# Performance work log

Measured on AMD Instinct MI355X. Metric: run time of the kernel, lower is better.

Reference implementation:

```python
import jax, jax.numpy as jnp
import numpy as np

INTERVAL = 0.5  # voxel_size_ratio
N_RAYS = 131072
M_SAMPLES = 8388608  # ~64 samples per ray on average
ALPHA_INIT = 0.01


def setup_inputs() -> dict:
    key = jax.random.key(0)
    k1, k2, k3 = jax.random.split(key, 3)
    density = jax.random.normal(k1, (M_SAMPLES,), jnp.float32)
    rgb_feat = jax.random.normal(k2, (M_SAMPLES, 3), jnp.float32)  # raw k0 colors
    # act_shift buffer: log(1/(1-alpha_init) - 1)
    shift = jnp.array([np.log(1.0 / (1.0 - ALPHA_INIT) - 1.0)], jnp.float32)
    # sorted ray ids (samples along each ray are contiguous, near->far)
    ray_id = jnp.sort(jax.random.randint(k3, (M_SAMPLES,), 0, N_RAYS)).astype(jnp.int32)
    return {"density": density, "rgb_feat": rgb_feat, "shift": shift,
            "ray_id": ray_id, "N": N_RAYS}


def reference(density, rgb_feat, shift, ray_id, N):
    # Raw2Alpha: alpha = 1 - (1 + exp(density + shift))^(-interval)
    #          = 1 - exp(-softplus(density + shift) * interval)
    sp = jax.nn.softplus(density + shift[0])
    log1ma = -sp * INTERVAL            # log(1 - alpha), exact
    alpha = 1.0 - jnp.exp(log1ma)

    # Alphas2Weights: per-ray exclusive cumulative product of (1 - alpha)
    # done in log space with a segmented exclusive cumsum.
    seg_tot = jax.ops.segment_sum(log1ma, ray_id, num_segments=N)   # [N] log prod per ray
    seg_excl = jnp.cumsum(seg_tot) - seg_tot                        # log prod of previous rays
    within_excl = jnp.cumsum(log1ma) - log1ma - seg_excl[ray_id]    # exclusive within segment
    T = jnp.exp(within_excl)          # transmittance before each sample
    weights = alpha * T               # [M]
    alphainv_last = jnp.exp(seg_tot)  # [N] leftover transmittance per ray

    # composite colors per ray + white-ish background via alphainv_last
    rgb = jax.nn.sigmoid(rgb_feat)
    rgb_marched = jax.ops.segment_sum(weights[:, None] * rgb, ray_id, num_segments=N)
    out = rgb_marched + alphainv_last[:, None]   # [N, 3]
    return weights, alphainv_last, out
```

## Files before the change

kernel.cpp:

```cpp
#include <hip/hip_runtime.h>


__device__ __forceinline__ float fast_sigmoid(float x) {
    return __builtin_amdgcn_rcpf(1.0f + __expf(-x));
}

#define DPP_ADD(x, ctrl, rmask)                                               \
    do {                                                                      \
        int _s = __builtin_amdgcn_update_dpp(0, __float_as_int(x), (ctrl),    \
                                             (rmask), 0xf, true);             \
        (x) += __int_as_float(_s);                                            \
    } while (0)

#define DPP_MUL(x, ctrl, rmask)                                               \
    do {                                                                      \
        int _s = __builtin_amdgcn_update_dpp(0x3f800000, __float_as_int(x),   \
                                             (ctrl), (rmask), 0xf, false);    \
        (x) *= __int_as_float(_s);                                            \
    } while (0)

__device__ __forceinline__ float wave_scan_add(float x) {
    DPP_ADD(x, 0x111, 0xf);
    DPP_ADD(x, 0x112, 0xf);
    DPP_ADD(x, 0x114, 0xf);
    DPP_ADD(x, 0x118, 0xf);
    DPP_ADD(x, 0x142, 0xa);
    DPP_ADD(x, 0x143, 0xc);
    return x;
}

__device__ __forceinline__ float wave_scan_mul(float x) {
    DPP_MUL(x, 0x111, 0xf);
    DPP_MUL(x, 0x112, 0xf);
    DPP_MUL(x, 0x114, 0xf);
    DPP_MUL(x, 0x118, 0xf);
    DPP_MUL(x, 0x142, 0xa);
    DPP_MUL(x, 0x143, 0xc);
    return x;
}

__device__ __forceinline__ float bcast_lane63(float x) {
    return __int_as_float(__builtin_amdgcn_readlane(__float_as_int(x), 63));
}

__global__ __launch_bounds__(256) void seg_starts4_kernel(
    const int4* __restrict__ ray4, int M4, int M, int N,
    const int* __restrict__ ray_id, int* __restrict__ starts)
{
    const int i = blockIdx.x * blockDim.x + threadIdx.x;
    if (i >= M4) return;
    const int4 v = ray4[i];
    const int prev = (i == 0) ? -1 : ray_id[4 * i - 1];
    const int base = 4 * i;
    for (int r = prev + 1; r <= v.x; ++r) starts[r] = base;
    for (int r = v.x + 1;  r <= v.y; ++r) starts[r] = base + 1;
    for (int r = v.y + 1;  r <= v.z; ++r) starts[r] = base + 2;
    for (int r = v.z + 1;  r <= v.w; ++r) starts[r] = base + 3;
    if (i == M4 - 1) {
        int last = v.w;
        for (int j = 4 * M4; j < M; ++j) {
            const int cur = ray_id[j];
            for (int r = last + 1; r <= cur; ++r) starts[r] = j;
            last = cur;
        }
        for (int r = last + 1; r <= N; ++r) starts[r] = M;
    }
}

#define RPW 4

__global__ __launch_bounds__(256, 4) void favor_render_kernel(
    const float* __restrict__ density,
    const float* __restrict__ rgb_feat,
    const float* __restrict__ shift,
    const int*   __restrict__ starts,
    int M, int N,
    float* __restrict__ weights,
    float* __restrict__ alphainv_last,
    float* __restrict__ out3)
{
    const int wave = (blockIdx.x * blockDim.x + threadIdx.x) >> 6;
    const int t    = threadIdx.x & 63;
    const int r0   = wave * RPW;
    if (r0 >= N) return;

    const int bv = starts[min(r0 + t, N)];
    int s[RPW + 1];
    #pragma unroll
    for (int k = 0; k <= RPW; ++k)
        s[k] = __builtin_amdgcn_readlane(bv, k);

    const float sh = shift[0];

    float d0[RPW], r0v[RPW], g0v[RPW], b0v[RPW];
    float d1[RPW], r1v[RPW], g1v[RPW], b1v[RPW];
    #pragma unroll
    for (int j = 0; j < RPW; ++j) {
        const int st = s[j], en = s[j + 1];
        const int c0 = max(min(st + t, en - 1), 0);
        d0[j]  = density[c0];
        r0v[j] = rgb_feat[3 * c0 + 0];
        g0v[j] = rgb_feat[3 * c0 + 1];
        b0v[j] = rgb_feat[3 * c0 + 2];
    }
    #pragma unroll
    for (int j = 0; j < RPW; ++j) {
        const int st = s[j], en = s[j + 1];
        const int c1 = max(min(st + 64 + t, en - 1), 0);
        d1[j]  = density[c1];
        r1v[j] = rgb_feat[3 * c1 + 0];
        g1v[j] = rgb_feat[3 * c1 + 1];
        b1v[j] = rgb_feat[3 * c1 + 2];
    }
    __builtin_amdgcn_sched_barrier(0);

    float carryT[RPW], accR[RPW], accG[RPW], accB[RPW];

    #pragma unroll
    for (int j = 0; j < RPW; ++j) {
        const int st = s[j], en = s[j + 1];
        const bool valid = (st + t) < en;
        const float u = 1.0f + __expf(d0[j] + sh);
        const float a = __builtin_amdgcn_rsqf(u);
        const float m = valid ? a : 1.0f;
        const float S = wave_scan_mul(m);
        carryT[j] = bcast_lane63(S);
        const float w = S * (u * a - 1.0f);
        accR[j] = valid ? w * fast_sigmoid(r0v[j]) : 0.0f;
        accG[j] = valid ? w * fast_sigmoid(g0v[j]) : 0.0f;
        accB[j] = valid ? w * fast_sigmoid(b0v[j]) : 0.0f;
        if (valid) weights[st + t] = w;
    }

    #pragma unroll
    for (int j = 0; j < RPW; ++j) {
        const int st = s[j], en = s[j + 1];
        if (en - st > 64) {
            const int i = st + 64 + t;
            const bool valid = i < en;
            const float u = 1.0f + __expf(d1[j] + sh);
            const float a = __builtin_amdgcn_rsqf(u);
            const float m = valid ? a : 1.0f;
            const float S = wave_scan_mul(m);
            const float tot = bcast_lane63(S);
            const float w = carryT[j] * S * (u * a - 1.0f);
            accR[j] += valid ? w * fast_sigmoid(r1v[j]) : 0.0f;
            accG[j] += valid ? w * fast_sigmoid(g1v[j]) : 0.0f;
            accB[j] += valid ? w * fast_sigmoid(b1v[j]) : 0.0f;
            if (valid) weights[i] = w;
            carryT[j] *= tot;

            for (int base = st + 128; base < en; base += 64) {
                const int ii = base + t;
                const bool v2 = ii < en;
                const int c = min(ii, en - 1);
                const float dd = density[c];
                const float rr = rgb_feat[3 * c + 0];
                const float gg = rgb_feat[3 * c + 1];
                const float bb = rgb_feat[3 * c + 2];
                const float u2 = 1.0f + __expf(dd + sh);
                const float a2 = __builtin_amdgcn_rsqf(u2);
                const float m2 = v2 ? a2 : 1.0f;
                const float S2 = wave_scan_mul(m2);
                const float tot2 = bcast_lane63(S2);
                const float w2 = carryT[j] * S2 * (u2 * a2 - 1.0f);
                if (v2) {
                    weights[ii] = w2;
                    accR[j] += w2 * fast_sigmoid(rr);
                    accG[j] += w2 * fast_sigmoid(gg);
                    accB[j] += w2 * fast_sigmoid(bb);
                }
                carryT[j] *= tot2;
            }
        }
    }

    float tR[RPW], tG[RPW], tB[RPW];
    #pragma unroll
    for (int j = 0; j < RPW; ++j) {
        tR[j] = wave_scan_add(accR[j]);
        tG[j] = wave_scan_add(accG[j]);
        tB[j] = wave_scan_add(accB[j]);
    }
    #pragma unroll
    for (int j = 0; j < RPW; ++j) {
        const float sR = bcast_lane63(tR[j]);
        const float sG = bcast_lane63(tG[j]);
        const float sB = bcast_lane63(tB[j]);
        const int ray = r0 + j;
        if (t == 0 && ray < N) {
            alphainv_last[ray] = carryT[j];
            out3[3 * ray + 0] = sR + carryT[j];
            out3[3 * ray + 1] = sG + carryT[j];
            out3[3 * ray + 2] = sB + carryT[j];
        }
    }
}

extern "C" void kernel_launch(void* const* d_in, const int* in_sizes, int n_in,
                              void* d_out, int out_size, void* d_ws, size_t ws_size,
                              hipStream_t stream) {
    const float* density  = (const float*)d_in[0];
    const float* rgb_feat = (const float*)d_in[1];
    const float* shift    = (const float*)d_in[2];
    const int*   ray_id   = (const int*)d_in[3];

    const int M = in_sizes[0];
    const int N = (out_size - M) / 4;

    float* weights       = (float*)d_out;
    float* alphainv_last = weights + M;
    float* out3          = alphainv_last + N;

    const int block = 256;
    int* starts = (int*)d_ws;

    const int M4 = M >> 2;
    const int grid_starts = (M4 + block - 1) / block;
    seg_starts4_kernel<<<grid_starts, block, 0, stream>>>(
        (const int4*)ray_id, M4, M, N, ray_id, starts);

    const int n_waves = (N + RPW - 1) / RPW;
    const int grid_render = (n_waves * 64 + block - 1) / block;
    favor_render_kernel<<<grid_render, block, 0, stream>>>(
        density, rgb_feat, shift, starts, M, N,
        weights, alphainv_last, out3);
}
```

Measured before the change: 208.5 us.

## Pack second-chunk samples of two rays into one wave using half-wave scans

New measurement: 213.5 us. +2.4%, slower.

```diff
diff --git a/kernel.cpp b/kernel.cpp
--- a/kernel.cpp
+++ b/kernel.cpp
@@ -39,8 +39,20 @@
     return x;
 }
 
+__device__ __forceinline__ float wave_scan_mul_half(float x) {
+    DPP_MUL(x, 0x111, 0xf);
+    DPP_MUL(x, 0x112, 0xf);
+    DPP_MUL(x, 0x114, 0xf);
+    DPP_MUL(x, 0x118, 0xf);
+    DPP_MUL(x, 0x142, 0xa);
+    return x;
+}
+
 __device__ __forceinline__ float bcast_lane63(float x) {
     return __int_as_float(__builtin_amdgcn_readlane(__float_as_int(x), 63));
+}
+__device__ __forceinline__ float bcast_lane31(float x) {
+    return __int_as_float(__builtin_amdgcn_readlane(__float_as_int(x), 31));
 }
 
 __global__ __launch_bounds__(256) void seg_starts4_kernel(
@@ -68,6 +80,7 @@
 }
 
 #define RPW 4
+#define NPAIR (RPW / 2)
 
 __global__ __launch_bounds__(256, 4) void favor_render_kernel(
     const float* __restrict__ density,
@@ -91,9 +104,9 @@
         s[k] = __builtin_amdgcn_readlane(bv, k);
 
     const float sh = shift[0];
+    const bool lowHalf = t < 32;
 
     float d0[RPW], r0v[RPW], g0v[RPW], b0v[RPW];
-    float d1[RPW], r1v[RPW], g1v[RPW], b1v[RPW];
     #pragma unroll
     for (int j = 0; j < RPW; ++j) {
         const int st = s[j], en = s[j + 1];
@@ -103,16 +116,19 @@
         g0v[j] = rgb_feat[3 * c0 + 1];
         b0v[j] = rgb_feat[3 * c0 + 2];
     }
-    #pragma unroll
-    for (int j = 0; j < RPW; ++j) {
-        const int st = s[j], en = s[j + 1];
-        const int c1 = max(min(st + 64 + t, en - 1), 0);
-        d1[j]  = density[c1];
-        r1v[j] = rgb_feat[3 * c1 + 0];
-        g1v[j] = rgb_feat[3 * c1 + 1];
-        b1v[j] = rgb_feat[3 * c1 + 2];
-    }
-    __builtin_amdgcn_sched_barrier(0);
+    float dP[NPAIR], rP[NPAIR], gP[NPAIR], bP[NPAIR];
+    int   iP[NPAIR];
+    #pragma unroll
+    for (int p = 0; p < NPAIR; ++p) {
+        const int idx = lowHalf ? (s[2 * p] + 64 + t) : (s[2 * p + 1] + 32 + t);
+        const int en  = lowHalf ? s[2 * p + 1] : s[2 * p + 2];
+        iP[p] = idx;
+        const int c = max(min(idx, en - 1), 0);
+        dP[p] = density[c];
+        rP[p] = rgb_feat[3 * c + 0];
+        gP[p] = rgb_feat[3 * c + 1];
+        bP[p] = rgb_feat[3 * c + 2];
+    }
 
     float carryT[RPW], accR[RPW], accG[RPW], accB[RPW];
 
@@ -133,27 +149,41 @@
     }
 
     #pragma unroll
+    for (int p = 0; p < NPAIR; ++p) {
+        const int jA = 2 * p, jB = 2 * p + 1;
+        const int en  = lowHalf ? s[jA + 1] : s[jB + 1];
+        const int idx = iP[p];
+        const bool valid = idx < en;
+        const float u = 1.0f + __expf(dP[p] + sh);
+        const float a = __builtin_amdgcn_rsqf(u);
+        const float m = valid ? a : 1.0f;
+        const float S = wave_scan_mul_half(m);
+        const float totA = bcast_lane31(S);
+        const float totB = bcast_lane63(S);
+        const float carrySel = lowHalf ? carryT[jA] : carryT[jB];
+        const float w = carrySel * S * (u * a - 1.0f);
+        const float cR = valid ? w * fast_sigmoid(rP[p]) : 0.0f;
+        const float cG = valid ? w * fast_sigmoid(gP[p]) : 0.0f;
+        const float cB = valid ? w * fast_sigmoid(bP[p]) : 0.0f;
+        accR[jA] += lowHalf ? cR : 0.0f;
+        accG[jA] += lowHalf ? cG : 0.0f;
+        accB[jA] += lowHalf ? cB : 0.0f;
+        accR[jB] += lowHalf ? 0.0f : cR;
+        accG[jB] += lowHalf ? 0.0f : cG;
+        accB[jB] += lowHalf ? 0.0f : cB;
+        if (valid) weights[idx] = w;
+        carryT[jA] *= totA;
+        carryT[jB] *= totB;
+    }
+
+    #pragma unroll
     for (int j = 0; j < RPW; ++j) {
         const int st = s[j], en = s[j + 1];
-        if (en - st > 64) {
-            const int i = st + 64 + t;
-            const bool valid = i < en;
-            const float u = 1.0f + __expf(d1[j] + sh);
-            const float a = __builtin_amdgcn_rsqf(u);
-            const float m = valid ? a : 1.0f;
-            const float S = wave_scan_mul(m);
-            const float tot = bcast_lane63(S);
-            const float w = carryT[j] * S * (u * a - 1.0f);
-            accR[j] += valid ? w * fast_sigmoid(r1v[j]) : 0.0f;
-            accG[j] += valid ? w * fast_sigmoid(g1v[j]) : 0.0f;
-            accB[j] += valid ? w * fast_sigmoid(b1v[j]) : 0.0f;
-            if (valid) weights[i] = w;
-            carryT[j] *= tot;
-
-            for (int base = st + 128; base < en; base += 64) {
-                const int ii = base + t;
-                const bool v2 = ii < en;
-                const int c = min(ii, en - 1);
+        if (en - st > 96) {
+            for (int base = st + 96; base < en; base += 64) {
+                const int i = base + t;
+                const bool v2 = i < en;
+                const int c = min(i, en - 1);
                 const float dd = density[c];
                 const float rr = rgb_feat[3 * c + 0];
                 const float gg = rgb_feat[3 * c + 1];
@@ -165,7 +195,7 @@
                 const float tot2 = bcast_lane63(S2);
                 const float w2 = carryT[j] * S2 * (u2 * a2 - 1.0f);
                 if (v2) {
-                    weights[ii] = w2;
+                    weights[i] = w2;
                     accR[j] += w2 * fast_sigmoid(rr);
                     accG[j] += w2 * fast_sigmoid(gg);
                     accB[j] += w2 * fast_sigmoid(bb);
```

## Process two samples per lane in first 128-sample chunk with single scan

Applied to the files above, without the earlier changes.

Result: no change. 210.8 us (+1.1%).

```diff
diff --git a/kernel.cpp b/kernel.cpp
--- a/kernel.cpp
+++ b/kernel.cpp
@@ -4,6 +4,9 @@
 __device__ __forceinline__ float fast_sigmoid(float x) {
     return __builtin_amdgcn_rcpf(1.0f + __expf(-x));
 }
+
+struct __align__(4) f3 { float x, y, z; };
+struct __align__(4) f2 { float x, y; };
 
 #define DPP_ADD(x, ctrl, rmask)                                               \
     do {                                                                      \
@@ -37,6 +40,12 @@
     DPP_MUL(x, 0x142, 0xa);
     DPP_MUL(x, 0x143, 0xc);
     return x;
+}
+
+__device__ __forceinline__ float dpp_excl_from_incl(float x) {
+    int r = __builtin_amdgcn_update_dpp(0x3f800000, __float_as_int(x),
+                                        0x138, 0xf, 0xf, false);
+    return __int_as_float(r);
 }
 
 __device__ __forceinline__ float bcast_lane63(float x) {
@@ -92,72 +101,66 @@
 
     const float sh = shift[0];
 
-    float d0[RPW], r0v[RPW], g0v[RPW], b0v[RPW];
-    float d1[RPW], r1v[RPW], g1v[RPW], b1v[RPW];
+    float dA[RPW], dB[RPW];
+    f3 cA[RPW], cB[RPW];
     #pragma unroll
     for (int j = 0; j < RPW; ++j) {
         const int st = s[j], en = s[j + 1];
-        const int c0 = max(min(st + t, en - 1), 0);
-        d0[j]  = density[c0];
-        r0v[j] = rgb_feat[3 * c0 + 0];
-        g0v[j] = rgb_feat[3 * c0 + 1];
-        b0v[j] = rgb_feat[3 * c0 + 2];
-    }
+        const int i0 = st + 2 * t;
+        const int c0 = max(min(i0,     en - 1), 0);
+        const int c1 = max(min(i0 + 1, en - 1), 0);
+        dA[j] = density[c0];
+        dB[j] = density[c1];
+        cA[j] = *(const f3*)(rgb_feat + 3 * c0);
+        cB[j] = *(const f3*)(rgb_feat + 3 * c1);
+    }
+
+    float carryT[RPW], accR[RPW], accG[RPW], accB[RPW];
+
     #pragma unroll
     for (int j = 0; j < RPW; ++j) {
         const int st = s[j], en = s[j + 1];
-        const int c1 = max(min(st + 64 + t, en - 1), 0);
-        d1[j]  = density[c1];
-        r1v[j] = rgb_feat[3 * c1 + 0];
-        g1v[j] = rgb_feat[3 * c1 + 1];
-        b1v[j] = rgb_feat[3 * c1 + 2];
-    }
-    __builtin_amdgcn_sched_barrier(0);
-
-    float carryT[RPW], accR[RPW], accG[RPW], accB[RPW];
+        const int i0 = st + 2 * t;
+        const bool v0 = i0 < en;
+        const bool v1 = (i0 + 1) < en;
+
+        const float u0 = 1.0f + __expf(dA[j] + sh);
+        const float u1 = 1.0f + __expf(dB[j] + sh);
+        const float a0r = __builtin_amdgcn_rsqf(u0);
+        const float a1r = __builtin_amdgcn_rsqf(u1);
+        const float a0 = v0 ? a0r : 1.0f;
+        const float a1 = v1 ? a1r : 1.0f;
+        const float m  = a0 * a1;
+
+        const float S = wave_scan_mul(m);
+        const float E = dpp_excl_from_incl(S);
+        carryT[j] = bcast_lane63(S);
+
+        const float w0 = E * (1.0f - a0);
+        const float w1 = (E * a0) * (1.0f - a1);
+
+        accR[j] = w0 * fast_sigmoid(cA[j].x) + w1 * fast_sigmoid(cB[j].x);
+        accG[j] = w0 * fast_sigmoid(cA[j].y) + w1 * fast_sigmoid(cB[j].y);
+        accB[j] = w0 * fast_sigmoid(cA[j].z) + w1 * fast_sigmoid(cB[j].z);
+
+        if (v1) {
+            f2 wv; wv.x = w0; wv.y = w1;
+            *(f2*)(weights + i0) = wv;
+        } else if (v0) {
+            weights[i0] = w0;
+        }
+    }
 
     #pragma unroll
     for (int j = 0; j < RPW; ++j) {
         const int st = s[j], en = s[j + 1];
-        const bool valid = (st + t) < en;
-        const float u = 1.0f + __expf(d0[j] + sh);
-        const float a = __builtin_amdgcn_rsqf(u);
-        const float m = valid ? a : 1.0f;
-        const float S = wave_scan_mul(m);
-        carryT[j] = bcast_lane63(S);
-        const float w = S * (u * a - 1.0f);
-        accR[j] = valid ? w * fast_sigmoid(r0v[j]) : 0.0f;
-        accG[j] = valid ? w * fast_sigmoid(g0v[j]) : 0.0f;
-        accB[j] = valid ? w * fast_sigmoid(b0v[j]) : 0.0f;
-        if (valid) weights[st + t] = w;
-    }
-
-    #pragma unroll
-    for (int j = 0; j < RPW; ++j) {
-        const int st = s[j], en = s[j + 1];
-        if (en - st > 64) {
-            const int i = st + 64 + t;
-            const bool valid = i < en;
-            const float u = 1.0f + __expf(d1[j] + sh);
-            const float a = __builtin_amdgcn_rsqf(u);
-            const float m = valid ? a : 1.0f;
-            const float S = wave_scan_mul(m);
-            const float tot = bcast_lane63(S);
-            const float w = carryT[j] * S * (u * a - 1.0f);
-            accR[j] += valid ? w * fast_sigmoid(r1v[j]) : 0.0f;
-            accG[j] += valid ? w * fast_sigmoid(g1v[j]) : 0.0f;
-            accB[j] += valid ? w * fast_sigmoid(b1v[j]) : 0.0f;
-            if (valid) weights[i] = w;
-            carryT[j] *= tot;
-
+        if (en - st > 128) {
             for (int base = st + 128; base < en; base += 64) {
-                const int ii = base + t;
-                const bool v2 = ii < en;
-                const int c = min(ii, en - 1);
+                const int i = base + t;
+                const bool v2 = i < en;
+                const int c = min(i, en - 1);
                 const float dd = density[c];
-                const float rr = rgb_feat[3 * c + 0];
-                const float gg = rgb_feat[3 * c + 1];
-                const float bb = rgb_feat[3 * c + 2];
+                const f3 cc = *(const f3*)(rgb_feat + 3 * c);
                 const float u2 = 1.0f + __expf(dd + sh);
                 const float a2 = __builtin_amdgcn_rsqf(u2);
                 const float m2 = v2 ? a2 : 1.0f;
@@ -165,34 +168,37 @@
                 const float tot2 = bcast_lane63(S2);
                 const float w2 = carryT[j] * S2 * (u2 * a2 - 1.0f);
                 if (v2) {
-                    weights[ii] = w2;
-                    accR[j] += w2 * fast_sigmoid(rr);
-                    accG[j] += w2 * fast_sigmoid(gg);
-                    accB[j] += w2 * fast_sigmoid(bb);
+                    weights[i] = w2;
+                    accR[j] += w2 * fast_sigmoid(cc.x);
+                    accG[j] += w2 * fast_sigmoid(cc.y);
+                    accB[j] += w2 * fast_sigmoid(cc.z);
                 }
                 carryT[j] *= tot2;
             }
         }
     }
 
-    float tR[RPW], tG[RPW], tB[RPW];
-    #pragma unroll
-    for (int j = 0; j < RPW; ++j) {
-        tR[j] = wave_scan_add(accR[j]);
-        tG[j] = wave_scan_add(accG[j]);
-        tB[j] = wave_scan_add(accB[j]);
-    }
-    #pragma unroll
-    for (int j = 0; j < RPW; ++j) {
-        const float sR = bcast_lane63(tR[j]);
-        const float sG = bcast_lane63(tG[j]);
-        const float sB = bcast_lane63(tB[j]);
-        const int ray = r0 + j;
-        if (t == 0 && ray < N) {
-            alphainv_last[ray] = carryT[j];
-            out3[3 * ray + 0] = sR + carryT[j];
-            out3[3 * ray + 1] = sG + carryT[j];
-            out3[3 * ray + 2] = sB + carryT[j];
+    float sR[RPW], sG[RPW], sB[RPW];
+    #pragma unroll
+    for (int j = 0; j < RPW; ++j) {
+        sR[j] = bcast_lane63(wave_scan_add(accR[j]));
+        sG[j] = bcast_lane63(wave_scan_add(accG[j]));
+        sB[j] = bcast_lane63(wave_scan_add(accB[j]));
+    }
+    if (t < RPW) {
+        const int ray = r0 + t;
+        if (ray < N) {
+            const float vT = (t == 0) ? carryT[0] : (t == 1) ? carryT[1]
+                           : (t == 2) ? carryT[2] : carryT[3];
+            const float vR = (t == 0) ? sR[0] : (t == 1) ? sR[1]
+                           : (t == 2) ? sR[2] : sR[3];
+            const float vG = (t == 0) ? sG[0] : (t == 1) ? sG[1]
+                           : (t == 2) ? sG[2] : sG[3];
+            const float vB = (t == 0) ? sB[0] : (t == 1) ? sB[1]
+                           : (t == 2) ? sB[2] : sB[3];
+            alphainv_last[ray] = vT;
+            f3 o; o.x = vR + vT; o.y = vG + vT; o.z = vB + vT;
+            *(f3*)(out3 + 3 * ray) = o;
         }
     }
 }
```
